# Optimization experiments

Hardware: AMD Instinct MI355X
Metric: run time of the kernel (lower is better)

The kernel has to match this reference:

```python
import jax, jax.numpy as jnp
import numpy as np

GROUP_SIZE = 8
REQUIRED_ZEROS = 4


def _dorefa_quantize(x, bits):
    # tanh-normalize-round
    t = jnp.tanh(x).astype(jnp.float32)
    y = t / jnp.max(jnp.abs(t))
    delta = float(2 ** (bits - 1) - 1)
    _y = jnp.round(y * delta)

    out_c, in_c, h, w = _y.shape
    if in_c < GROUP_SIZE:
        return _y / delta

    g = in_c // GROUP_SIZE
    keep = GROUP_SIZE - REQUIRED_ZEROS  # keep at most 4 non-zeros per group

    # [out_c, g*8, h, w] -> [out_c, g, h, w, 8] (group axis last for top_k)
    yg = _y[:, : g * GROUP_SIZE].reshape(out_c, g, GROUP_SIZE, h, w)
    yg = jnp.transpose(yg, (0, 1, 3, 4, 2))

    # The torch loop zeroes the smallest-|v| non-zeros until >=4 zeros per
    # group. Equivalently: keep only the `keep` largest-|v| entries of each
    # group (zeros have |v|=0, so groups already having >=4 zeros are
    # unchanged). Fully vectorized via batched top-k + one-hot mask.
    absv = jnp.abs(yg)
    _, idx = jax.lax.top_k(absv, keep)                      # [o,g,h,w,keep]
    mask = jax.nn.one_hot(idx, GROUP_SIZE, dtype=yg.dtype).sum(axis=-2)
    yg = yg * mask                                          # [o,g,h,w,8]

    yg = jnp.transpose(yg, (0, 1, 4, 2, 3)).reshape(out_c, g * GROUP_SIZE, h, w)
    out = jnp.concatenate([yg, _y[:, g * GROUP_SIZE :]], axis=1) if g * GROUP_SIZE < in_c else yg
    return out / delta


def setup_inputs() -> dict:
    key = jax.random.key(0)
    x = jax.random.normal(key, (2048, 2048, 3, 3), dtype=jnp.float32)
    return {"x": x, "bits": 8}


def reference(x, bits):
    return _dorefa_quantize(x, bits)
```

## Files before the change

### kernel.cpp

```cpp
#include <hip/hip_runtime.h>
#include <math.h>

#define HW        9
#define GROUP     8
#define KEEP      4
#define DELTA     127.0f
#define INV_DELTA (1.0f / 127.0f)
#define GB_FLOATS 72

#define GB_TILE   32
#define TILE_F    (GB_TILE * GB_FLOATS)
#define TILE_CH   (TILE_F / 256)
#define CELLS     (GB_TILE * HW)
#define WPB       4
#define NT        4

typedef float f32x4 __attribute__((ext_vector_type(4)));

__device__ __forceinline__ unsigned umx(unsigned a, unsigned b) { return a > b ? a : b; }
__device__ __forceinline__ unsigned umn(unsigned a, unsigned b) { return a < b ? a : b; }

__global__ void maxabs_kernel(const float4* __restrict__ x, unsigned* __restrict__ ws, int n4) {
    __shared__ float red[4];
    float m = 0.0f;
    int stride = gridDim.x * blockDim.x;
    #pragma unroll 4
    for (int i = blockIdx.x * blockDim.x + threadIdx.x; i < n4; i += stride) {
        float4 v = x[i];
        m = fmaxf(m, fmaxf(fmaxf(fabsf(v.x), fabsf(v.y)),
                           fmaxf(fabsf(v.z), fabsf(v.w))));
    }
    #pragma unroll
    for (int off = 32; off > 0; off >>= 1)
        m = fmaxf(m, __shfl_down(m, off, 64));
    int wave = threadIdx.x >> 6;
    if ((threadIdx.x & 63) == 0) red[wave] = m;
    __syncthreads();
    if (threadIdx.x == 0) {
        float b = fmaxf(fmaxf(red[0], red[1]), fmaxf(red[2], red[3]));
        atomicMax(ws, __float_as_uint(b));
    }
}

__device__ __attribute__((noinline)) float ref_rz(float xx, float M) {
    float td = (float)tanh((double)xx);
    float y  = td / M;
    return rintf(y * DELTA);
}

__device__ __forceinline__ float fast_tanh(float x) {
    float ax  = fabsf(x);
    float axc = fminf(ax, 10.0f);
    float E   = __expf(2.0f * axc);
    float num = E - 1.0f;
    float den = E + 1.0f;
    float r0  = __builtin_amdgcn_rcpf(den);
    float r   = r0 * fmaf(-den, r0, 2.0f);
    float tl  = copysignf(num * r, x);
    float s = x * x;
    float p = fmaf(s, 0.0035921280f, -0.0088632358f);
    p = fmaf(s, p, 0.021869488f);
    p = fmaf(s, p, -0.053968254f);
    p = fmaf(s, p, 0.13333334f);
    p = fmaf(s, p, -0.33333334f);
    float ts = fmaf(x * s, p, x);
    return (ax <= 0.5f) ? ts : tl;
}

__device__ __forceinline__ void compute_tile(float* ldsw, int lane, float M, float C) {
    #pragma unroll
    for (int c = 0; c < (CELLS + 63) / 64; ++c) {
        int ci = lane + 64 * c;
        if (ci < CELLS) {
            int gb = ci / 9;
            int hw = ci - gb * 9;
            float* cell = ldsw + gb * GB_FLOATS + hw;

            float v8[GROUP];
            unsigned K[GROUP];
            #pragma unroll
            for (int j = 0; j < GROUP; ++j) {
                float xx = cell[9 * j];
                float t  = fast_tanh(xx);
                float z  = t * C;
                float rz = rintf(z);
                float d  = 0.5f - fabsf(z - rz);
                if (d < fmaf(2e-6f, fabsf(z), 5e-7f))
                    rz = ref_rz(xx, M);
                v8[j] = rz;
                K[j] = ((unsigned)fabsf(rz) << 3) | (unsigned)(7 - j);
            }

            unsigned s0 = K[0], s1 = K[1], s2 = K[2], s3 = K[3];
            unsigned s4 = K[4], s5 = K[5], s6 = K[6], s7 = K[7];
            #define CE_(x, y) { unsigned _h = umx(x, y), _l = umn(x, y); x = _h; y = _l; }
            CE_(s0, s1) CE_(s2, s3) CE_(s0, s2) CE_(s1, s3) CE_(s1, s2)
            CE_(s4, s5) CE_(s6, s7) CE_(s4, s6) CE_(s5, s7) CE_(s5, s6)
            #undef CE_
            unsigned T = umx(umx(umn(s0, s6), umn(s1, s5)),
                             umx(umn(s2, s4), umx(s3, s7)));

            #pragma unroll
            for (int j = 0; j < GROUP; ++j)
                cell[9 * j] = (K[j] >= T) ? (v8[j] * INV_DELTA) : 0.0f;
        }
    }
}

__global__ __launch_bounds__(256, 3) void quant_kernel(const float* __restrict__ x,
                             float* __restrict__ out,
                             const unsigned* __restrict__ ws,
                             int n_gb) {
    __shared__ float lds[WPB][TILE_F];
    __shared__ float sM, sC;
    if (threadIdx.x == 0) {
        float mm = (float)tanh((double)__uint_as_float(*ws));
        sM = mm;
        sC = (float)(127.0 / (double)mm);
    }
    __syncthreads();
    float M = sM, C = sC;

    const int wv   = threadIdx.x >> 6;
    const int lane = threadIdx.x & 63;
    const int wave_id = blockIdx.x * WPB + wv;

    const size_t tbase0 = (size_t)wave_id * NT * TILE_F;
    float* ldsw = &lds[wv][0];
    f32x4* l4 = (f32x4*)ldsw;

    f32x4 ra[TILE_CH], rb[TILE_CH];

    {
        const f32x4* s4 = (const f32x4*)(x + tbase0);
        #pragma unroll
        for (int k = 0; k < TILE_CH; ++k) ra[k] = s4[k * 64 + lane];
    }

    #pragma unroll
    for (int i = 0; i < NT; ++i) {
        f32x4* cur = (i & 1) ? rb : ra;
        f32x4* nxt = (i & 1) ? ra : rb;

        if (i + 1 < NT) {
            const f32x4* sn = (const f32x4*)(x + tbase0 + (size_t)(i + 1) * TILE_F);
            #pragma unroll
            for (int k = 0; k < TILE_CH; ++k) nxt[k] = sn[k * 64 + lane];
        }
        __builtin_amdgcn_sched_barrier(0);

        #pragma unroll
        for (int k = 0; k < TILE_CH; ++k) l4[k * 64 + lane] = cur[k];
        __builtin_amdgcn_sched_barrier(0);

        compute_tile(ldsw, lane, M, C);
        __builtin_amdgcn_sched_barrier(0);

        f32x4* dst4 = (f32x4*)(out + tbase0 + (size_t)i * TILE_F);
        #pragma unroll
        for (int k = 0; k < TILE_CH; ++k)
            dst4[k * 64 + lane] = l4[k * 64 + lane];
        __builtin_amdgcn_sched_barrier(0);
    }
}

extern "C" void kernel_launch(void* const* d_in, const int* in_sizes, int n_in,
                              void* d_out, int out_size, void* d_ws, size_t ws_size,
                              hipStream_t stream) {
    const float* x = (const float*)d_in[0];
    float* out = (float*)d_out;
    unsigned* ws = (unsigned*)d_ws;

    int n = in_sizes[0];
    int n4 = n / 4;
    int n_gb = n / GB_FLOATS;

    hipMemsetAsync(ws, 0, sizeof(unsigned), stream);

    maxabs_kernel<<<2048, 256, 0, stream>>>((const float4*)x, ws, n4);

    int blocks_q = n_gb / (GB_TILE * NT * WPB);
    quant_kernel<<<blocks_q, 256, 0, stream>>>(x, out, ws, n_gb);
}
```

Measured before the change: 305.6 us.

## Replace LDS-staged tiled quant kernel with direct per-cell global access kernel

Drops the wave-level LDS staging with register double-buffering and has each thread handle one (group, hw) cell, reading its 8 strided values straight from global memory and writing them back directly. The per-block tanh/scale computation moves into a separate single-thread prep kernel that stores M and C in the workspace. This removes LDS traffic and the serial per-block tanh, and allows higher occupancy, but uses stride-9 uncoalesced global accesses that depend on the cache to merge, and adds one kernel launch.

```diff
diff --git a/kernel.cpp b/kernel.cpp
--- a/kernel.cpp
+++ b/kernel.cpp
@@ -7,18 +7,6 @@
 #define DELTA     127.0f
 #define INV_DELTA (1.0f / 127.0f)
 #define GB_FLOATS 72
-
-#define GB_TILE   32
-#define TILE_F    (GB_TILE * GB_FLOATS)
-#define TILE_CH   (TILE_F / 256)
-#define CELLS     (GB_TILE * HW)
-#define WPB       4
-#define NT        4
-
-typedef float f32x4 __attribute__((ext_vector_type(4)));
-
-__device__ __forceinline__ unsigned umx(unsigned a, unsigned b) { return a > b ? a : b; }
-__device__ __forceinline__ unsigned umn(unsigned a, unsigned b) { return a < b ? a : b; }
 
 __global__ void maxabs_kernel(const float4* __restrict__ x, unsigned* __restrict__ ws, int n4) {
     __shared__ float red[4];
@@ -39,6 +27,14 @@
     if (threadIdx.x == 0) {
         float b = fmaxf(fmaxf(red[0], red[1]), fmaxf(red[2], red[3]));
         atomicMax(ws, __float_as_uint(b));
+    }
+}
+
+__global__ void prep_kernel(unsigned* __restrict__ ws) {
+    if (threadIdx.x == 0) {
+        double mm = tanh((double)__uint_as_float(ws[0]));
+        ws[1] = __float_as_uint((float)mm);
+        ws[2] = __float_as_uint((float)(127.0 / mm));
     }
 }
 
@@ -67,101 +63,52 @@
     return (ax <= 0.5f) ? ts : tl;
 }
 
-__device__ __forceinline__ void compute_tile(float* ldsw, int lane, float M, float C) {
+__device__ __forceinline__ unsigned umx(unsigned a, unsigned b) { return a > b ? a : b; }
+__device__ __forceinline__ unsigned umn(unsigned a, unsigned b) { return a < b ? a : b; }
+
+__global__ __launch_bounds__(256, 6) void quant_cell(const float* __restrict__ x,
+                                                     float* __restrict__ out,
+                                                     const unsigned* __restrict__ ws,
+                                                     int n_cells) {
+    int ci = blockIdx.x * 256 + threadIdx.x;
+    if (ci >= n_cells) return;
+
+    const float M = __uint_as_float(ws[1]);
+    const float C = __uint_as_float(ws[2]);
+
+    int gb = ci / 9;
+    int hw = ci - gb * 9;
+    const size_t base = (size_t)gb * GB_FLOATS + hw;
+    const float* px = x + base;
+
+    float v8[GROUP];
+    unsigned K[GROUP];
     #pragma unroll
-    for (int c = 0; c < (CELLS + 63) / 64; ++c) {
-        int ci = lane + 64 * c;
-        if (ci < CELLS) {
-            int gb = ci / 9;
-            int hw = ci - gb * 9;
-            float* cell = ldsw + gb * GB_FLOATS + hw;
-
-            float v8[GROUP];
-            unsigned K[GROUP];
-            #pragma unroll
-            for (int j = 0; j < GROUP; ++j) {
-                float xx = cell[9 * j];
-                float t  = fast_tanh(xx);
-                float z  = t * C;
-                float rz = rintf(z);
-                float d  = 0.5f - fabsf(z - rz);
-                if (d < fmaf(2e-6f, fabsf(z), 5e-7f))
-                    rz = ref_rz(xx, M);
-                v8[j] = rz;
-                K[j] = ((unsigned)fabsf(rz) << 3) | (unsigned)(7 - j);
-            }
-
-            unsigned s0 = K[0], s1 = K[1], s2 = K[2], s3 = K[3];
-            unsigned s4 = K[4], s5 = K[5], s6 = K[6], s7 = K[7];
-            #define CE_(x, y) { unsigned _h = umx(x, y), _l = umn(x, y); x = _h; y = _l; }
-            CE_(s0, s1) CE_(s2, s3) CE_(s0, s2) CE_(s1, s3) CE_(s1, s2)
-            CE_(s4, s5) CE_(s6, s7) CE_(s4, s6) CE_(s5, s7) CE_(s5, s6)
-            #undef CE_
-            unsigned T = umx(umx(umn(s0, s6), umn(s1, s5)),
-                             umx(umn(s2, s4), umx(s3, s7)));
-
-            #pragma unroll
-            for (int j = 0; j < GROUP; ++j)
-                cell[9 * j] = (K[j] >= T) ? (v8[j] * INV_DELTA) : 0.0f;
-        }
-    }
-}
-
-__global__ __launch_bounds__(256, 3) void quant_kernel(const float* __restrict__ x,
-                             float* __restrict__ out,
-                             const unsigned* __restrict__ ws,
-                             int n_gb) {
-    __shared__ float lds[WPB][TILE_F];
-    __shared__ float sM, sC;
-    if (threadIdx.x == 0) {
-        float mm = (float)tanh((double)__uint_as_float(*ws));
-        sM = mm;
-        sC = (float)(127.0 / (double)mm);
-    }
-    __syncthreads();
-    float M = sM, C = sC;
-
-    const int wv   = threadIdx.x >> 6;
-    const int lane = threadIdx.x & 63;
-    const int wave_id = blockIdx.x * WPB + wv;
-
-    const size_t tbase0 = (size_t)wave_id * NT * TILE_F;
-    float* ldsw = &lds[wv][0];
-    f32x4* l4 = (f32x4*)ldsw;
-
-    f32x4 ra[TILE_CH], rb[TILE_CH];
-
-    {
-        const f32x4* s4 = (const f32x4*)(x + tbase0);
-        #pragma unroll
-        for (int k = 0; k < TILE_CH; ++k) ra[k] = s4[k * 64 + lane];
+    for (int j = 0; j < GROUP; ++j) {
+        float xx = px[9 * j];
+        float t  = fast_tanh(xx);
+        float z  = t * C;
+        float rz = rintf(z);
+        float d  = 0.5f - fabsf(z - rz);
+        if (d < fmaf(2e-6f, fabsf(z), 5e-7f))
+            rz = ref_rz(xx, M);
+        v8[j] = rz;
+        K[j] = ((unsigned)fabsf(rz) << 3) | (unsigned)(7 - j);
     }
 
+    unsigned s0 = K[0], s1 = K[1], s2 = K[2], s3 = K[3];
+    unsigned s4 = K[4], s5 = K[5], s6 = K[6], s7 = K[7];
+    #define CE_(a, b) { unsigned _h = umx(a, b), _l = umn(a, b); a = _h; b = _l; }
+    CE_(s0, s1) CE_(s2, s3) CE_(s0, s2) CE_(s1, s3) CE_(s1, s2)
+    CE_(s4, s5) CE_(s6, s7) CE_(s4, s6) CE_(s5, s7) CE_(s5, s6)
+    #undef CE_
+    unsigned T = umx(umx(umn(s0, s6), umn(s1, s5)),
+                     umx(umn(s2, s4), umx(s3, s7)));
+
+    float* po = out + base;
     #pragma unroll
-    for (int i = 0; i < NT; ++i) {
-        f32x4* cur = (i & 1) ? rb : ra;
-        f32x4* nxt = (i & 1) ? ra : rb;
-
-        if (i + 1 < NT) {
-            const f32x4* sn = (const f32x4*)(x + tbase0 + (size_t)(i + 1) * TILE_F);
-            #pragma unroll
-            for (int k = 0; k < TILE_CH; ++k) nxt[k] = sn[k * 64 + lane];
-        }
-        __builtin_amdgcn_sched_barrier(0);
-
-        #pragma unroll
-        for (int k = 0; k < TILE_CH; ++k) l4[k * 64 + lane] = cur[k];
-        __builtin_amdgcn_sched_barrier(0);
-
-        compute_tile(ldsw, lane, M, C);
-        __builtin_amdgcn_sched_barrier(0);
-
-        f32x4* dst4 = (f32x4*)(out + tbase0 + (size_t)i * TILE_F);
-        #pragma unroll
-        for (int k = 0; k < TILE_CH; ++k)
-            dst4[k * 64 + lane] = l4[k * 64 + lane];
-        __builtin_amdgcn_sched_barrier(0);
-    }
+    for (int j = 0; j < GROUP; ++j)
+        po[9 * j] = (K[j] >= T) ? (v8[j] * INV_DELTA) : 0.0f;
 }
 
 extern "C" void kernel_launch(void* const* d_in, const int* in_sizes, int n_in,
@@ -173,12 +120,13 @@
 
     int n = in_sizes[0];
     int n4 = n / 4;
-    int n_gb = n / GB_FLOATS;
+    int n_cells = n / GROUP;
 
     hipMemsetAsync(ws, 0, sizeof(unsigned), stream);
 
     maxabs_kernel<<<2048, 256, 0, stream>>>((const float4*)x, ws, n4);
+    prep_kernel<<<1, 64, 0, stream>>>(ws);
 
-    int blocks_q = n_gb / (GB_TILE * NT * WPB);
-    quant_kernel<<<blocks_q, 256, 0, stream>>>(x, out, ws, n_gb);
+    int blocks_q = (n_cells + 255) / 256;
+    quant_cell<<<blocks_q, 256, 0, stream>>>(x, out, ws, n_cells);
 }
```

After: 310.9 us. About the same (+1.7%).
